# Performance work log

Measured on AMD Instinct MI355X. Metric: run time of the kernel, lower is better.

The kernel has to match this reference:

```python
import math
import jax, jax.numpy as jnp
from jax import lax
import numpy as np

B, S, D = 4, 128, 256          # batch, image side (l_max = S*S), d_model
FO = 64                        # filter_order (MLP width)
EMB = 3                        # emb_dim (time + 1 band sine/cosine)
FAST, SLOW, TARGET = 0.3, 1.5, 0.01


def setup_inputs() -> dict:
    key = jax.random.key(0)
    ks = jax.random.split(key, 20)
    d3 = 3 * D
    def rn(k, shp, scale):
        return jax.random.normal(k, shp, jnp.float32) * scale
    inp = {
        "x": jax.random.normal(ks[0], (B, S * S, D), jnp.float32),
        # in_proj / out_proj
        "in_w": rn(ks[1], (D, d3), 1.0 / math.sqrt(D)),
        "in_b": jnp.zeros((d3,), jnp.float32),
        "out_w": rn(ks[2], (D, D), 1.0 / math.sqrt(D)),
        "out_b": jnp.zeros((D,), jnp.float32),
        # depthwise 3x3 short filter
        "sf_w": rn(ks[3], (d3, 1, 3, 3), 1.0 / 3.0),
        "sf_b": jnp.zeros((d3,), jnp.float32),
        # Sin activation frequency (shared across all Sin uses; w=1, train_freq=True)
        "freq": jnp.ones((1, FO), jnp.float32),
        # X implicit filter MLP: Linear(3,FO) -> Sin -> Linear(FO,FO) -> Sin -> Linear(FO,FO) -> Sin -> Linear(FO,D,no bias)
        "xw0": rn(ks[4], (EMB, FO), 0.5), "xb0": jnp.zeros((FO,), jnp.float32),
        "xw1": rn(ks[5], (FO, FO), 1.0 / math.sqrt(FO)), "xb1": jnp.zeros((FO,), jnp.float32),
        "xw2": rn(ks[6], (FO, FO), 1.0 / math.sqrt(FO)), "xb2": jnp.zeros((FO,), jnp.float32),
        "xw3": rn(ks[7], (FO, D), 1.0 / math.sqrt(FO)),
        # Y implicit filter MLP (same structure)
        "yw0": rn(ks[8], (EMB, FO), 0.5), "yb0": jnp.zeros((FO,), jnp.float32),
        "yw1": rn(ks[9], (FO, FO), 1.0 / math.sqrt(FO)), "yb1": jnp.zeros((FO,), jnp.float32),
        "yw2": rn(ks[10], (FO, FO), 1.0 / math.sqrt(FO)), "yb2": jnp.zeros((FO,), jnp.float32),
        "yw3": rn(ks[11], (FO, D), 1.0 / math.sqrt(FO)),
        # HyenaFilter2d residual bias D (torch: randn)
        "fbias": jax.random.normal(ks[12], (D,), jnp.float32),
    }
    return inp


def _pos_emb():
    # PositionalEmbedding with emb_dim=3 -> bands=1
    t = jnp.linspace(0.0, 1.0, S)[None, :, None]                 # (1,S,1)
    tr = jnp.linspace(0.0, S - 1.0, S)[None, :, None]
    w_ang = 2.0 * math.pi * tr / S
    f = jnp.linspace(1e-4, 0.0, 1)[None, None]                   # bands=1
    zc = jnp.exp(-1j * f * w_ang)                                # (1,S,1) complex
    z = jnp.concatenate([t, zc.real, zc.imag], axis=-1)          # (1,S,3)
    return z.astype(jnp.float32), t.astype(jnp.float32)


def _decay(t):
    max_d = math.log(TARGET) / FAST
    min_d = math.log(TARGET) / SLOW
    deltas = jnp.linspace(min_d, max_d, D)[None, None]           # (1,1,D) buffer
    return jnp.exp(-t * jnp.abs(deltas))                         # (1,S,D)


def _mlp(z, freq, w0, b0, w1, b1, w2, b2, w3):
    h = jnp.sin(freq * (z @ w0 + b0))
    h = jnp.sin(freq * (h @ w1 + b1))
    h = jnp.sin(freq * (h @ w2 + b2))
    return h @ w3                                                # (1,S,D)


def _fftconv2d(u, k, Db):
    # u: (B,D,S,S), k: (D,S,S), Db: (D,)
    n = 2 * S
    kf = jnp.fft.rfft2(k.astype(jnp.float32), s=(n, n)) / n
    uf = jnp.fft.rfft2(u.astype(jnp.float32), s=(n, n))
    y = jnp.fft.irfft2(uf * kf, s=(n, n))[..., :S, :S]
    return y + u * Db[None, :, None, None]


def reference(x, in_w, in_b, out_w, out_b, sf_w, sf_b, freq,
              xw0, xb0, xw1, xb1, xw2, xb2, xw3,
              yw0, yb0, yw1, yb1, yw2, yb2, yw3, fbias):
    d3 = 3 * D
    # projection and reshape to 2D grid: b (h w) c -> b c h w
    u = x @ in_w + in_b                                          # (B,L,3D)
    u = u.reshape(B, S, S, d3).transpose(0, 3, 1, 2)             # (B,3D,S,S)
    # depthwise 3x3 short filter, padding=2, crop to S (matches Conv padding=2 + [:S])
    uc = lax.conv_general_dilated(u, sf_w, (1, 1), ((2, 2), (2, 2)),
                                  feature_group_count=d3,
                                  dimension_numbers=("NCHW", "OIHW", "NCHW"))
    uc = uc[..., :S, :S] + sf_b[None, :, None, None]
    x0, x1, v = jnp.split(uc, 3, axis=1)                         # each (B,D,S,S)
    # implicit separable 2D filter
    z, t = _pos_emb()
    dec = _decay(t)
    hx = _mlp(z, freq, xw0, xb0, xw1, xb1, xw2, xb2, xw3) * dec  # (1,S,D)
    hy = _mlp(z, freq, yw0, yb0, yw1, yb1, yw2, yb2, yw3) * dec
    k = jnp.einsum('ijk,imk->ijmk', hx, hy)[0]                   # (S,S,D)
    k = jnp.transpose(k, (2, 0, 1))                              # (D,S,S)
    # hyena recurrence (order=2): single gated fft conv
    v = v * x1
    v = _fftconv2d(v, k, fbias)
    y = v * x0
    y = y.transpose(0, 2, 3, 1).reshape(B, S * S, D)             # b c h w -> b (h w) c
    return y @ out_w + out_b
```

## Files before the change

### kernel.cpp

```cpp
#include <hip/hip_runtime.h>
#include <hip/hip_bf16.h>

#define S_DIM 128
#define B_DIM 4
#define L_DIM (S_DIM * S_DIM)

typedef __bf16 bf16x8 __attribute__((ext_vector_type(8)));
typedef float f32x4 __attribute__((ext_vector_type(4)));

__device__ __forceinline__ float b2f(unsigned short u) {
    union { unsigned int i; float f; } v;
    v.i = ((unsigned int)u) << 16;
    return v.f;
}
__device__ __forceinline__ unsigned short f2b(float f) {
    union { float f; unsigned int i; } v;
    v.f = f;
    unsigned int x = v.i;
    return (unsigned short)((x + 0x7FFFu + ((x >> 16) & 1u)) >> 16);
}
__device__ __forceinline__ float ldx(const void* p, size_t i, int f32) {
    return f32 ? ((const float*)p)[i] : b2f(((const unsigned short*)p)[i]);
}

__global__ __launch_bounds__(256) void sniff_dtype(const unsigned short* __restrict__ x,
                                                   int* __restrict__ flag) {
    __shared__ int cnt;
    if (threadIdx.x == 0) cnt = 0;
    __syncthreads();
    int c = 0;
    for (int i = threadIdx.x; i < 32768; i += 256) {
        unsigned int e = (x[i] >> 7) & 0xFFu;
        if (e >= 0x91u) c++;
    }
    atomicAdd(&cnt, c);
    __syncthreads();
    if (threadIdx.x == 0) flag[0] = (cnt > 64) ? 1 : 0;
}

__global__ void transpose_any(const void* __restrict__ src,
                              unsigned short* __restrict__ dst, int R, int C,
                              const int* __restrict__ flag) {
    const int f = flag[0];
    int idx = blockIdx.x * 256 + threadIdx.x;
    if (idx >= R * C) return;
    int r = idx / C, c = idx - r * C;
    dst[c * R + r] = f2b(ldx(src, idx, f));
}

__global__ __launch_bounds__(256) void filter_mlp(
    const void* __restrict__ freq,
    const void* __restrict__ w0, const void* __restrict__ b0,
    const void* __restrict__ w1, const void* __restrict__ b1,
    const void* __restrict__ w2, const void* __restrict__ b2,
    const void* __restrict__ w3,
    float* __restrict__ out, const int* __restrict__ flag)
{
    __shared__ float hs[64], gs[64];
    const int f32f = flag[0];
    const int s   = blockIdx.x;
    const int tid = threadIdx.x;
    const float t = (float)s / (float)(S_DIM - 1);
    const float ang = 1e-4f * 2.0f * 3.14159265358979323846f * ((float)s / (float)S_DIM);
    const float z0 = t, z1 = cosf(ang), z2 = -sinf(ang);

    if (tid < 64) {
        float fr = ldx(freq, tid, f32f);
        float a = z0 * ldx(w0, 0 * 64 + tid, f32f) + z1 * ldx(w0, 1 * 64 + tid, f32f) +
                  z2 * ldx(w0, 2 * 64 + tid, f32f) + ldx(b0, tid, f32f);
        hs[tid] = sinf(fr * a);
    }
    __syncthreads();
    if (tid < 64) {
        float fr = ldx(freq, tid, f32f);
        float a = ldx(b1, tid, f32f);
        for (int e = 0; e < 64; e++) a += hs[e] * ldx(w1, e * 64 + tid, f32f);
        gs[tid] = sinf(fr * a);
    }
    __syncthreads();
    if (tid < 64) {
        float fr = ldx(freq, tid, f32f);
        float a = ldx(b2, tid, f32f);
        for (int e = 0; e < 64; e++) a += gs[e] * ldx(w2, e * 64 + tid, f32f);
        hs[tid] = sinf(fr * a);
    }
    __syncthreads();
    {
        const float min_d = -3.0701134573253943f;
        const float max_d = -15.350567286626971f;
        float a = 0.f;
        for (int e = 0; e < 64; e++) a += hs[e] * ldx(w3, e * 256 + tid, f32f);
        float delta = min_d + (max_d - min_d) * ((float)tid / 255.0f);
        float dec = expf(-t * fabsf(delta));
        out[s * 256 + tid] = a * dec;
    }
}

__global__ __launch_bounds__(256) void gemm_bt(
    const void* __restrict__ A, size_t a_off, int a_ext,
    const unsigned short* __restrict__ BT,
    const void* __restrict__ bias, int bias_ext,
    void* __restrict__ C, size_t c_off, int c_ext,
    int M, int N, int K, const int* __restrict__ flag)
{
    __shared__ unsigned short As[128 * 40];
    __shared__ unsigned short Bs[128 * 40];

    const int f     = flag[0];
    const int a_f32 = a_ext && f;
    const int b_f32 = bias_ext && f;
    const int c_f32 = c_ext && f;

    const int tid  = threadIdx.x;
    const int m0   = blockIdx.x * 128;
    const int n0   = blockIdx.y * 128;
    const int wid  = tid >> 6;
    const int lane = tid & 63;
    const int lrow = lane & 15;
    const int quad = lane >> 4;
    const int wr   = wid >> 1, wc = wid & 1;

    f32x4 acc[4][4];
#pragma unroll
    for (int a = 0; a < 4; a++)
#pragma unroll
        for (int b = 0; b < 4; b++)
#pragma unroll
            for (int r = 0; r < 4; r++) acc[a][b][r] = 0.0f;

    for (int kc = 0; kc < K; kc += 32) {
#pragma unroll
        for (int h = 0; h < 2; h++) {
            int c    = tid + h * 256;
            int row  = c >> 2;
            int col8 = (c & 3) * 8;
            size_t aidx = a_off + (size_t)(m0 + row) * K + kc + col8;
            if (a_f32) {
                const float4* ga = (const float4*)((const float*)A + aidx);
                float4 p0 = ga[0], p1 = ga[1];
                uint4 w;
                w.x = (unsigned int)f2b(p0.x) | ((unsigned int)f2b(p0.y) << 16);
                w.y = (unsigned int)f2b(p0.z) | ((unsigned int)f2b(p0.w) << 16);
                w.z = (unsigned int)f2b(p1.x) | ((unsigned int)f2b(p1.y) << 16);
                w.w = (unsigned int)f2b(p1.z) | ((unsigned int)f2b(p1.w) << 16);
                *(uint4*)(&As[row * 40 + col8]) = w;
            } else {
                *(uint4*)(&As[row * 40 + col8]) =
                    *(const uint4*)((const unsigned short*)A + aidx);
            }
            *(uint4*)(&Bs[row * 40 + col8]) =
                *(const uint4*)(BT + (size_t)(n0 + row) * K + kc + col8);
        }
        __syncthreads();

        bf16x8 af[4], bfr[4];
#pragma unroll
        for (int fm = 0; fm < 4; fm++)
            af[fm] = *(const bf16x8*)(&As[(wr * 64 + fm * 16 + lrow) * 40 + quad * 8]);
#pragma unroll
        for (int fn = 0; fn < 4; fn++)
            bfr[fn] = *(const bf16x8*)(&Bs[(wc * 64 + fn * 16 + lrow) * 40 + quad * 8]);
#pragma unroll
        for (int fm = 0; fm < 4; fm++)
#pragma unroll
            for (int fn = 0; fn < 4; fn++)
                acc[fm][fn] = __builtin_amdgcn_mfma_f32_16x16x32_bf16(
                    af[fm], bfr[fn], acc[fm][fn], 0, 0, 0);
        __syncthreads();
    }

#pragma unroll
    for (int fm = 0; fm < 4; fm++) {
#pragma unroll
        for (int fn = 0; fn < 4; fn++) {
            int gcol = n0 + wc * 64 + fn * 16 + lrow;
            float bv = ldx(bias, gcol, b_f32);
#pragma unroll
            for (int r = 0; r < 4; r++) {
                int grow = m0 + wr * 64 + fm * 16 + quad * 4 + r;
                size_t cidx = c_off + (size_t)grow * N + gcol;
                float val = acc[fm][fn][r] + bv;
                if (c_f32) ((float*)C)[cidx] = val;
                else       ((unsigned short*)C)[cidx] = f2b(val);
            }
        }
    }
}

__global__ __launch_bounds__(192) void conv3_gate(
    const unsigned short* __restrict__ U, size_t u_zs,
    const void* __restrict__ sfw, const void* __restrict__ sfb,
    unsigned short* __restrict__ Wb, unsigned short* __restrict__ X0, size_t o_zs,
    const int* __restrict__ flag)
{
    __shared__ __align__(16) float x1f[2][256];

    const int f32f = flag[0];
    const int i    = blockIdx.x;
    const int j0   = blockIdx.y * 32;
    const int tid  = threadIdx.x;
    const int wv   = tid >> 6;
    const int lane = tid & 63;
    const int ch0  = wv * 256 + lane * 4;

    const unsigned short* Ub = U + (size_t)blockIdx.z * u_zs;
    unsigned short* Wbb = Wb + (size_t)blockIdx.z * o_zs;
    unsigned short* X0b = X0 + (size_t)blockIdx.z * o_zs;

    float wgt[3][3][4], bias[4];
#pragma unroll
    for (int c = 0; c < 4; c++) {
        int ch = ch0 + c;
        bias[c] = ldx(sfb, ch, f32f);
#pragma unroll
        for (int ki = 0; ki < 3; ki++)
#pragma unroll
            for (int kj = 0; kj < 3; kj++)
                wgt[ki][kj][c] = ldx(sfw, ch * 9 + ki * 3 + kj, f32f);
    }

    bool rok[3];
    const unsigned short* rp[3];
#pragma unroll
    for (int ki = 0; ki < 3; ki++) {
        int row = i + ki - 2;
        rok[ki] = (row >= 0);
        rp[ki]  = Ub + (size_t)(row * S_DIM) * 768 + ch0;
    }

    float win[3][3][4];
#define DLOAD(slot, col)                                                       \
    { _Pragma("unroll") for (int ki = 0; ki < 3; ki++) {                       \
        if (rok[ki] && (col) >= 0) {                                           \
            uint2 p = *(const uint2*)(rp[ki] + (size_t)(col) * 768);           \
            win[slot][ki][0] = b2f((unsigned short)p.x);                       \
            win[slot][ki][1] = b2f((unsigned short)(p.x >> 16));               \
            win[slot][ki][2] = b2f((unsigned short)p.y);                       \
            win[slot][ki][3] = b2f((unsigned short)(p.y >> 16));               \
        } else {                                                               \
            win[slot][ki][0] = 0.f; win[slot][ki][1] = 0.f;                    \
            win[slot][ki][2] = 0.f; win[slot][ki][3] = 0.f;                    \
        } } }

    DLOAD(0, j0 - 2)
    DLOAD(1, j0 - 1)

    uint2 nxt[3];
#pragma unroll
    for (int ki = 0; ki < 3; ki++) {
        uint2 p; p.x = 0u; p.y = 0u;
        if (rok[ki]) p = *(const uint2*)(rp[ki] + (size_t)j0 * 768);
        nxt[ki] = p;
    }

#pragma unroll
    for (int jj = 0; jj < 32; jj++) {
        const int j  = j0 + jj;
        const int sA = jj % 3, sB = (jj + 1) % 3, sC = (jj + 2) % 3;

#pragma unroll
        for (int ki = 0; ki < 3; ki++) {
            win[sC][ki][0] = b2f((unsigned short)nxt[ki].x);
            win[sC][ki][1] = b2f((unsigned short)(nxt[ki].x >> 16));
            win[sC][ki][2] = b2f((unsigned short)nxt[ki].y);
            win[sC][ki][3] = b2f((unsigned short)(nxt[ki].y >> 16));
        }
        {
            const int jn = j + 1;
            const bool jok = (jn < S_DIM);
#pragma unroll
            for (int ki = 0; ki < 3; ki++) {
                uint2 p; p.x = 0u; p.y = 0u;
                if (jok && rok[ki]) p = *(const uint2*)(rp[ki] + (size_t)jn * 768);
                nxt[ki] = p;
            }
        }

        float o[4];
#pragma unroll
        for (int c = 0; c < 4; c++) {
            float a = bias[c];
#pragma unroll
            for (int ki = 0; ki < 3; ki++)
                a += wgt[ki][0][c] * win[sA][ki][c]
                   + wgt[ki][1][c] * win[sB][ki][c]
                   + wgt[ki][2][c] * win[sC][ki][c];
            o[c] = a;
        }

        const size_t oidx = (size_t)(i * S_DIM + j) * 256 + lane * 4;
        if (wv == 1) {
            float4 v4; v4.x = o[0]; v4.y = o[1]; v4.z = o[2]; v4.w = o[3];
            *(float4*)(&x1f[jj & 1][lane * 4]) = v4;
        } else if (wv == 0) {
            unsigned int lo = (unsigned int)f2b(o[0]) | ((unsigned int)f2b(o[1]) << 16);
            unsigned int hi = (unsigned int)f2b(o[2]) | ((unsigned int)f2b(o[3]) << 16);
            uint2 st; st.x = lo; st.y = hi;
            *(uint2*)(&X0b[oidx]) = st;
        }
        __syncthreads();
        if (wv == 2) {
            float4 xp = *(const float4*)(&x1f[jj & 1][lane * 4]);
            float r0 = o[0] * xp.x;
            float r1 = o[1] * xp.y;
            float r2 = o[2] * xp.z;
            float r3 = o[3] * xp.w;
            unsigned int lo = (unsigned int)f2b(r0) | ((unsigned int)f2b(r1) << 16);
            unsigned int hi = (unsigned int)f2b(r2) | ((unsigned int)f2b(r3) << 16);
            uint2 st; st.x = lo; st.y = hi;
            *(uint2*)(&Wbb[oidx]) = st;
        }
    }
#undef DLOAD
}

__global__ __launch_bounds__(256) void conv_j(
    const unsigned short* __restrict__ Wb, size_t zs,
    const float* __restrict__ hy,
    unsigned short* __restrict__ Aout)
{
    __shared__ unsigned short wl[S_DIM * 256];
    const int i = blockIdx.x;
    const int h = blockIdx.y;
    const int tid = threadIdx.x;
    const size_t zoff = (size_t)blockIdx.z * zs;
    const size_t sbase = zoff + (size_t)(i * S_DIM) * 256;

    const uint4* gsrc = (const uint4*)(Wb + sbase);
    for (int c = tid; c < 4096; c += 256) ((uint4*)wl)[c] = gsrc[c];
    __syncthreads();

    const int d = tid;
    const float* hyd = hy + d;

    for (int pick = 0; pick < 2; pick++) {
        const int jt = pick ? (7 - h) : h;
        const int j0 = jt * 16;
        float acc[16];
#pragma unroll
        for (int jj = 0; jj < 16; jj++) acc[jj] = 0.f;

        float ww[24];
#pragma unroll
        for (int t = 0; t < 24; t++) {
            int r = j0 + 15 - t;
            ww[t] = (r >= 0) ? b2f(wl[r * 256 + d]) : 0.f;
        }
        float hA[8], hB[8];
#pragma unroll
        for (int k = 0; k < 8; k++) hA[k] = hyd[k * 256];

        const int nbh = jt + 1;
        for (int bb = 0; bb < nbh; bb++) {
            const int q0 = 16 * bb;
            const bool last = (bb + 1 == nbh);
            float wn[8];
#pragma unroll
            for (int k = 0; k < 8; k++) hB[k] = hyd[(q0 + 8 + k) * 256];
#pragma unroll
            for (int k = 0; k < 8; k++) {
                int r = j0 - q0 - 9 - k;
                wn[k] = (r >= 0) ? b2f(wl[r * 256 + d]) : 0.f;
            }
#pragma unroll
            for (int k = 0; k < 8; k++)
#pragma unroll
                for (int jj = 0; jj < 16; jj++)
                    acc[jj] += hA[k] * ww[15 - jj + k];
#pragma unroll
            for (int t = 0; t < 16; t++) ww[t] = ww[t + 8];
#pragma unroll
            for (int k = 0; k < 8; k++) ww[16 + k] = wn[k];
            if (!last) {
#pragma unroll
                for (int k = 0; k < 8; k++) hA[k] = hyd[(q0 + 16 + k) * 256];
#pragma unroll
                for (int k = 0; k < 8; k++) {
                    int r = j0 - q0 - 17 - k;
                    wn[k] = (r >= 0) ? b2f(wl[r * 256 + d]) : 0.f;
                }
            }
#pragma unroll
            for (int k = 0; k < 8; k++)
#pragma unroll
                for (int jj = 0; jj < 16; jj++)
                    acc[jj] += hB[k] * ww[15 - jj + k];
            if (!last) {
#pragma unroll
                for (int t = 0; t < 16; t++) ww[t] = ww[t + 8];
#pragma unroll
                for (int k = 0; k < 8; k++) ww[16 + k] = wn[k];
            }
        }
#pragma unroll
        for (int jj = 0; jj < 16; jj++)
            Aout[sbase + (size_t)(j0 + jj) * 256 + d] = f2b(acc[jj]);
    }
}

__global__ __launch_bounds__(256) void conv_i(
    const unsigned short* __restrict__ Ain, size_t zs,
    const float* __restrict__ hx,
    const unsigned short* __restrict__ Wb,
    const unsigned short* __restrict__ X0,
    const void* __restrict__ fbias,
    unsigned short* __restrict__ Gout,
    const int* __restrict__ flag)
{
    __shared__ unsigned short al[S_DIM * 256];
    const int f32f = flag[0];
    const int j = blockIdx.x;
    const int h = blockIdx.y;
    const int tid = threadIdx.x;
    const size_t zoff = (size_t)blockIdx.z * zs;

    for (int c = tid; c < 4096; c += 256) {
        int row = c >> 5;
        int off = c & 31;
        const uint4* gsrc = (const uint4*)(Ain + zoff + (size_t)(row * S_DIM + j) * 256) + off;
        ((uint4*)al)[c] = *gsrc;
    }
    __syncthreads();

    const int d = tid;
    const float* hxd = hx + d;
    const float fb = ldx(fbias, d, f32f);

    for (int pick = 0; pick < 2; pick++) {
        const int it = pick ? (7 - h) : h;
        const int i0 = it * 16;
        float acc[16];
#pragma unroll
        for (int ii = 0; ii < 16; ii++) acc[ii] = 0.f;

        float ww[24];
#pragma unroll
        for (int t = 0; t < 24; t++) {
            int r = i0 + 15 - t;
            ww[t] = (r >= 0) ? b2f(al[r * 256 + d]) : 0.f;
        }
        float hA[8], hB[8];
#pragma unroll
        for (int k = 0; k < 8; k++) hA[k] = hxd[k * 256];

        const int nbh = it + 1;
        for (int bb = 0; bb < nbh; bb++) {
            const int q0 = 16 * bb;
            const bool last = (bb + 1 == nbh);
            float wn[8];
#pragma unroll
            for (int k = 0; k < 8; k++) hB[k] = hxd[(q0 + 8 + k) * 256];
#pragma unroll
            for (int k = 0; k < 8; k++) {
                int r = i0 - q0 - 9 - k;
                wn[k] = (r >= 0) ? b2f(al[r * 256 + d]) : 0.f;
            }
#pragma unroll
            for (int k = 0; k < 8; k++)
#pragma unroll
                for (int ii = 0; ii < 16; ii++)
                    acc[ii] += hA[k] * ww[15 - ii + k];
#pragma unroll
            for (int t = 0; t < 16; t++) ww[t] = ww[t + 8];
#pragma unroll
            for (int k = 0; k < 8; k++) ww[16 + k] = wn[k];
            if (!last) {
#pragma unroll
                for (int k = 0; k < 8; k++) hA[k] = hxd[(q0 + 16 + k) * 256];
#pragma unroll
                for (int k = 0; k < 8; k++) {
                    int r = i0 - q0 - 17 - k;
                    wn[k] = (r >= 0) ? b2f(al[r * 256 + d]) : 0.f;
                }
            }
#pragma unroll
            for (int k = 0; k < 8; k++)
#pragma unroll
                for (int ii = 0; ii < 16; ii++)
                    acc[ii] += hB[k] * ww[15 - ii + k];
            if (!last) {
#pragma unroll
                for (int t = 0; t < 16; t++) ww[t] = ww[t + 8];
#pragma unroll
                for (int k = 0; k < 8; k++) ww[16 + k] = wn[k];
            }
        }
#pragma unroll
        for (int ii = 0; ii < 16; ii++) {
            int i = i0 + ii;
            size_t idx = zoff + (size_t)(i * S_DIM + j) * 256 + d;
            float wv  = b2f(Wb[idx]);
            float x0v = b2f(X0[idx]);
            float y = acc[ii] * (1.0f / 256.0f) + wv * fb;
            Gout[idx] = f2b(y * x0v);
        }
    }
}

extern "C" void kernel_launch(void* const* d_in, const int* in_sizes, int n_in,
                              void* d_out, int out_size, void* d_ws, size_t ws_size,
                              hipStream_t stream)
{
    const void* x     = d_in[0];
    const void* in_w  = d_in[1];
    const void* in_b  = d_in[2];
    const void* out_w = d_in[3];
    const void* out_b_= d_in[4];
    const void* sf_w  = d_in[5];
    const void* sf_b  = d_in[6];
    const void* freq  = d_in[7];
    const void* xw0 = d_in[8];  const void* xb0 = d_in[9];
    const void* xw1 = d_in[10]; const void* xb1 = d_in[11];
    const void* xw2 = d_in[12]; const void* xb2 = d_in[13];
    const void* xw3 = d_in[14];
    const void* yw0 = d_in[15]; const void* yb0 = d_in[16];
    const void* yw1 = d_in[17]; const void* yb1 = d_in[18];
    const void* yw2 = d_in[19]; const void* yb2 = d_in[20];
    const void* yw3 = d_in[21];
    const void* fbias = d_in[22];

    char* ws = (char*)d_ws;
    const size_t UZ  = (size_t)L_DIM * 768;
    const size_t OZ  = (size_t)L_DIM * 256;

    const size_t need_fused = 168558608;
    bool fused = (ws_size >= need_fused);

    if (fused) {
        unsigned short* u_f  = (unsigned short*)(ws + 0);
        unsigned short* A_f  = (unsigned short*)(ws + 0);
        unsigned short* G_f  = (unsigned short*)(ws + 33554432);
        unsigned short* Wb_f = (unsigned short*)(ws + 100663296);
        unsigned short* X0_f = (unsigned short*)(ws + 134217728);
        float* hx            = (float*)(ws + 167772160);
        float* hy            = (float*)(ws + 167903232);
        unsigned short* tin  = (unsigned short*)(ws + 168034304);
        unsigned short* tout = (unsigned short*)(ws + 168427520);
        int* flag            = (int*)(ws + 168558592);

        sniff_dtype<<<1, 256, 0, stream>>>((const unsigned short*)x, flag);
        transpose_any<<<dim3(768), 256, 0, stream>>>(in_w, tin, 256, 768, flag);
        transpose_any<<<dim3(256), 256, 0, stream>>>(out_w, tout, 256, 256, flag);
        filter_mlp<<<dim3(S_DIM), 256, 0, stream>>>(freq, xw0, xb0, xw1, xb1, xw2, xb2, xw3, hx, flag);
        filter_mlp<<<dim3(S_DIM), 256, 0, stream>>>(freq, yw0, yb0, yw1, yb1, yw2, yb2, yw3, hy, flag);

        gemm_bt<<<dim3(512, 6), 256, 0, stream>>>(
            x, 0, 1, tin, in_b, 1, u_f, 0, 0, B_DIM * L_DIM, 768, 256, flag);
        conv3_gate<<<dim3(S_DIM, 4, B_DIM), 192, 0, stream>>>(
            u_f, UZ, sf_w, sf_b, Wb_f, X0_f, OZ, flag);
        conv_j<<<dim3(S_DIM, 4, B_DIM), 256, 0, stream>>>(Wb_f, OZ, hy, A_f);
        conv_i<<<dim3(S_DIM, 4, B_DIM), 256, 0, stream>>>(
            A_f, OZ, hx, Wb_f, X0_f, fbias, G_f, flag);
        gemm_bt<<<dim3(512, 2), 256, 0, stream>>>(
            G_f, 0, 0, tout, out_b_, 1, d_out, 0, 1, B_DIM * L_DIM, 256, 256, flag);
    } else {
        unsigned short* u_b  = (unsigned short*)(ws + 0);
        unsigned short* A_b  = (unsigned short*)(ws + 0);
        unsigned short* G_b  = (unsigned short*)(ws + 8388608);
        unsigned short* Wb_b = (unsigned short*)(ws + 25165824);
        unsigned short* X0_b = (unsigned short*)(ws + 33554432);
        float* hx            = (float*)(ws + 41943040);
        float* hy            = (float*)(ws + 42074112);
        unsigned short* tin  = (unsigned short*)(ws + 42205184);
        unsigned short* tout = (unsigned short*)(ws + 42598400);
        int* flag            = (int*)(ws + 42729472);

        sniff_dtype<<<1, 256, 0, stream>>>((const unsigned short*)x, flag);
        transpose_any<<<dim3(768), 256, 0, stream>>>(in_w, tin, 256, 768, flag);
        transpose_any<<<dim3(256), 256, 0, stream>>>(out_w, tout, 256, 256, flag);
        filter_mlp<<<dim3(S_DIM), 256, 0, stream>>>(freq, xw0, xb0, xw1, xb1, xw2, xb2, xw3, hx, flag);
        filter_mlp<<<dim3(S_DIM), 256, 0, stream>>>(freq, yw0, yb0, yw1, yb1, yw2, yb2, yw3, hy, flag);

        for (int b = 0; b < B_DIM; b++) {
            size_t xoff = (size_t)b * OZ;
            gemm_bt<<<dim3(128, 6), 256, 0, stream>>>(
                x, xoff, 1, tin, in_b, 1, u_b, 0, 0, L_DIM, 768, 256, flag);
            conv3_gate<<<dim3(S_DIM, 4, 1), 192, 0, stream>>>(
                u_b, 0, sf_w, sf_b, Wb_b, X0_b, 0, flag);
            conv_j<<<dim3(S_DIM, 4, 1), 256, 0, stream>>>(Wb_b, 0, hy, A_b);
            conv_i<<<dim3(S_DIM, 4, 1), 256, 0, stream>>>(
                A_b, 0, hx, Wb_b, X0_b, fbias, G_b, flag);
            gemm_bt<<<dim3(128, 2), 256, 0, stream>>>(
                G_b, 0, 0, tout, out_b_, 1, d_out, xoff, 1, L_DIM, 256, 256, flag);
        }
    }
}
```

Baseline: 552.4 us.

## Pre-cast input to bf16 and stage GEMM tiles with direct global-to-LDS loads

Adds a cast kernel that converts the fp32 input to bf16 once, so the input projection GEMM no longer converts fp32 on the fly six times, once per N-tile column. The GEMM now uses global_load_lds (16-byte direct global-to-LDS) with an unpadded 32-wide LDS row layout instead of register-staged stores into padded rows. The cost is an extra pass over the input (read fp32, write bf16) and possible LDS bank conflicts from dropping the padding.

```diff
diff --git a/kernel.cpp b/kernel.cpp
--- a/kernel.cpp
+++ b/kernel.cpp
@@ -21,6 +21,11 @@
 }
 __device__ __forceinline__ float ldx(const void* p, size_t i, int f32) {
     return f32 ? ((const float*)p)[i] : b2f(((const unsigned short*)p)[i]);
+}
+__device__ __forceinline__ void gload16(const unsigned short* g, unsigned short* l) {
+    __builtin_amdgcn_global_load_lds(
+        (const __attribute__((address_space(1))) unsigned int*)g,
+        (__attribute__((address_space(3))) unsigned int*)l, 16, 0, 0);
 }
 
 __global__ __launch_bounds__(256) void sniff_dtype(const unsigned short* __restrict__ x,
@@ -46,6 +51,31 @@
     if (idx >= R * C) return;
     int r = idx / C, c = idx - r * C;
     dst[c * R + r] = f2b(ldx(src, idx, f));
+}
+
+__global__ __launch_bounds__(256) void cast_to_bf16(
+    const void* __restrict__ src, size_t s_off,
+    unsigned short* __restrict__ dst, size_t n,
+    const int* __restrict__ flag)
+{
+    const int f = flag[0];
+    size_t idx = ((size_t)blockIdx.x * 256 + threadIdx.x) * 8;
+    const size_t stride = (size_t)gridDim.x * 256 * 8;
+    for (; idx < n; idx += stride) {
+        if (f) {
+            const float4* s4 = (const float4*)((const float*)src + s_off + idx);
+            float4 a = s4[0], b = s4[1];
+            uint4 w;
+            w.x = (unsigned int)f2b(a.x) | ((unsigned int)f2b(a.y) << 16);
+            w.y = (unsigned int)f2b(a.z) | ((unsigned int)f2b(a.w) << 16);
+            w.z = (unsigned int)f2b(b.x) | ((unsigned int)f2b(b.y) << 16);
+            w.w = (unsigned int)f2b(b.z) | ((unsigned int)f2b(b.w) << 16);
+            *(uint4*)(dst + idx) = w;
+        } else {
+            *(uint4*)(dst + idx) =
+                *(const uint4*)((const unsigned short*)src + s_off + idx);
+        }
+    }
 }
 
 __global__ __launch_bounds__(256) void filter_mlp(
@@ -96,18 +126,17 @@
     }
 }
 
-__global__ __launch_bounds__(256) void gemm_bt(
-    const void* __restrict__ A, size_t a_off, int a_ext,
+__global__ __launch_bounds__(256) void gemm_bt16(
+    const unsigned short* __restrict__ A,
     const unsigned short* __restrict__ BT,
     const void* __restrict__ bias, int bias_ext,
     void* __restrict__ C, size_t c_off, int c_ext,
     int M, int N, int K, const int* __restrict__ flag)
 {
-    __shared__ unsigned short As[128 * 40];
-    __shared__ unsigned short Bs[128 * 40];
+    __shared__ __align__(16) unsigned short As[128 * 32];
+    __shared__ __align__(16) unsigned short Bs[128 * 32];
 
     const int f     = flag[0];
-    const int a_f32 = a_ext && f;
     const int b_f32 = bias_ext && f;
     const int c_f32 = c_ext && f;
 
@@ -120,6 +149,9 @@
     const int quad = lane >> 4;
     const int wr   = wid >> 1, wc = wid & 1;
 
+    const int srow = lane >> 2;
+    const int scol = (lane & 3) * 8;
+
     f32x4 acc[4][4];
 #pragma unroll
     for (int a = 0; a < 4; a++)
@@ -130,36 +162,21 @@
 
     for (int kc = 0; kc < K; kc += 32) {
 #pragma unroll
-        for (int h = 0; h < 2; h++) {
-            int c    = tid + h * 256;
-            int row  = c >> 2;
-            int col8 = (c & 3) * 8;
-            size_t aidx = a_off + (size_t)(m0 + row) * K + kc + col8;
-            if (a_f32) {
-                const float4* ga = (const float4*)((const float*)A + aidx);
-                float4 p0 = ga[0], p1 = ga[1];
-                uint4 w;
-                w.x = (unsigned int)f2b(p0.x) | ((unsigned int)f2b(p0.y) << 16);
-                w.y = (unsigned int)f2b(p0.z) | ((unsigned int)f2b(p0.w) << 16);
-                w.z = (unsigned int)f2b(p1.x) | ((unsigned int)f2b(p1.y) << 16);
-                w.w = (unsigned int)f2b(p1.z) | ((unsigned int)f2b(p1.w) << 16);
-                *(uint4*)(&As[row * 40 + col8]) = w;
-            } else {
-                *(uint4*)(&As[row * 40 + col8]) =
-                    *(const uint4*)((const unsigned short*)A + aidx);
-            }
-            *(uint4*)(&Bs[row * 40 + col8]) =
-                *(const uint4*)(BT + (size_t)(n0 + row) * K + kc + col8);
+        for (int c = 0; c < 2; c++) {
+            const int ch  = wid * 2 + c;
+            const int row = ch * 16 + srow;
+            gload16(A  + (size_t)(m0 + row) * K + kc + scol, &As[ch * 512]);
+            gload16(BT + (size_t)(n0 + row) * K + kc + scol, &Bs[ch * 512]);
         }
         __syncthreads();
 
         bf16x8 af[4], bfr[4];
 #pragma unroll
         for (int fm = 0; fm < 4; fm++)
-            af[fm] = *(const bf16x8*)(&As[(wr * 64 + fm * 16 + lrow) * 40 + quad * 8]);
+            af[fm] = *(const bf16x8*)(&As[(wr * 64 + fm * 16 + lrow) * 32 + quad * 8]);
 #pragma unroll
         for (int fn = 0; fn < 4; fn++)
-            bfr[fn] = *(const bf16x8*)(&Bs[(wc * 64 + fn * 16 + lrow) * 40 + quad * 8]);
+            bfr[fn] = *(const bf16x8*)(&Bs[(wc * 64 + fn * 16 + lrow) * 32 + quad * 8]);
 #pragma unroll
         for (int fm = 0; fm < 4; fm++)
 #pragma unroll
@@ -532,6 +549,7 @@
         unsigned short* G_f  = (unsigned short*)(ws + 33554432);
         unsigned short* Wb_f = (unsigned short*)(ws + 100663296);
         unsigned short* X0_f = (unsigned short*)(ws + 134217728);
+        unsigned short* xb_f = (unsigned short*)(ws + 100663296);
         float* hx            = (float*)(ws + 167772160);
         float* hy            = (float*)(ws + 167903232);
         unsigned short* tin  = (unsigned short*)(ws + 168034304);
@@ -544,21 +562,24 @@
         filter_mlp<<<dim3(S_DIM), 256, 0, stream>>>(freq, xw0, xb0, xw1, xb1, xw2, xb2, xw3, hx, flag);
         filter_mlp<<<dim3(S_DIM), 256, 0, stream>>>(freq, yw0, yb0, yw1, yb1, yw2, yb2, yw3, hy, flag);
 
-        gemm_bt<<<dim3(512, 6), 256, 0, stream>>>(
-            x, 0, 1, tin, in_b, 1, u_f, 0, 0, B_DIM * L_DIM, 768, 256, flag);
+        cast_to_bf16<<<dim3(2048), 256, 0, stream>>>(
+            x, 0, xb_f, (size_t)B_DIM * L_DIM * 256, flag);
+        gemm_bt16<<<dim3(512, 6), 256, 0, stream>>>(
+            xb_f, tin, in_b, 1, u_f, 0, 0, B_DIM * L_DIM, 768, 256, flag);
         conv3_gate<<<dim3(S_DIM, 4, B_DIM), 192, 0, stream>>>(
             u_f, UZ, sf_w, sf_b, Wb_f, X0_f, OZ, flag);
         conv_j<<<dim3(S_DIM, 4, B_DIM), 256, 0, stream>>>(Wb_f, OZ, hy, A_f);
         conv_i<<<dim3(S_DIM, 4, B_DIM), 256, 0, stream>>>(
             A_f, OZ, hx, Wb_f, X0_f, fbias, G_f, flag);
-        gemm_bt<<<dim3(512, 2), 256, 0, stream>>>(
-            G_f, 0, 0, tout, out_b_, 1, d_out, 0, 1, B_DIM * L_DIM, 256, 256, flag);
+        gemm_bt16<<<dim3(512, 2), 256, 0, stream>>>(
+            G_f, tout, out_b_, 1, d_out, 0, 1, B_DIM * L_DIM, 256, 256, flag);
     } else {
         unsigned short* u_b  = (unsigned short*)(ws + 0);
         unsigned short* A_b  = (unsigned short*)(ws + 0);
         unsigned short* G_b  = (unsigned short*)(ws + 8388608);
         unsigned short* Wb_b = (unsigned short*)(ws + 25165824);
         unsigned short* X0_b = (unsigned short*)(ws + 33554432);
+        unsigned short* xb_b = (unsigned short*)(ws + 25165824);
         float* hx            = (float*)(ws + 41943040);
         float* hy            = (float*)(ws + 42074112);
         unsigned short* tin  = (unsigned short*)(ws + 42205184);
@@ -573,15 +594,17 @@
 
         for (int b = 0; b < B_DIM; b++) {
             size_t xoff = (size_t)b * OZ;
-            gemm_bt<<<dim3(128, 6), 256, 0, stream>>>(
-                x, xoff, 1, tin, in_b, 1, u_b, 0, 0, L_DIM, 768, 256, flag);
+            cast_to_bf16<<<dim3(2048), 256, 0, stream>>>(
+                x, xoff, xb_b, (size_t)L_DIM * 256, flag);
+            gemm_bt16<<<dim3(128, 6), 256, 0, stream>>>(
+                xb_b, tin, in_b, 1, u_b, 0, 0, L_DIM, 768, 256, flag);
             conv3_gate<<<dim3(S_DIM, 4, 1), 192, 0, stream>>>(
                 u_b, 0, sf_w, sf_b, Wb_b, X0_b, 0, flag);
             conv_j<<<dim3(S_DIM, 4, 1), 256, 0, stream>>>(Wb_b, 0, hy, A_b);
             conv_i<<<dim3(S_DIM, 4, 1), 256, 0, stream>>>(
                 A_b, 0, hx, Wb_b, X0_b, fbias, G_b, flag);
-            gemm_bt<<<dim3(128, 2), 256, 0, stream>>>(
-                G_b, 0, 0, tout, out_b_, 1, d_out, xoff, 1, L_DIM, 256, 256, flag);
-        }
-    }
-}
+            gemm_bt16<<<dim3(128, 2), 256, 0, stream>>>(
+                G_b, tout, out_b_, 1, d_out, xoff, 1, L_DIM, 256, 256, flag);
+        }
+    }
+}
```

Result: no change. 550.2 us (-0.4%).
